# Optimization experiments

Measured on AMD Instinct MI355X. Metric: run time of the kernel, lower is better.

## Reference

```python
import jax, jax.numpy as jnp
import numpy as np

B, C, HF, WF = 32, 512, 8, 64   # pre-extracted VGG feature map
S = HF * WF                      # encoder sequence length = 512
T = 128                          # decode steps
V = 512                          # vocab size
E = 128                          # embedding dim
EH = 256                         # encoder hidden (per direction)
DH = 256                         # decoder hidden


def _p(key, shape, scale=0.08):
    return jax.random.normal(key, shape, dtype=jnp.float32) * scale


def setup_inputs() -> dict:
    key = jax.random.key(0)
    ks = jax.random.split(key, 24)
    inp = {
        'source': jax.random.normal(ks[0], (B, C, HF, WF), jnp.float32),
        'target': jax.random.randint(ks[1], (B, T), 0, V),
        # encoder bidirectional GRU (1 layer, input 512, hidden 256)
        'enc_Wih_f': _p(ks[2], (3 * EH, C)), 'enc_Whh_f': _p(ks[3], (3 * EH, EH)),
        'enc_bih_f': _p(ks[4], (3 * EH,)),   'enc_bhh_f': _p(ks[5], (3 * EH,)),
        'enc_Wih_b': _p(ks[6], (3 * EH, C)), 'enc_Whh_b': _p(ks[7], (3 * EH, EH)),
        'enc_bih_b': _p(ks[8], (3 * EH,)),   'enc_bhh_b': _p(ks[9], (3 * EH,)),
        # location-based attention: Linear(2*EH + DH -> 1)
        'att_W': _p(ks[10], (1, 2 * EH + DH)), 'att_b': _p(ks[11], (1,)),
        # decoder embedding
        'emb': _p(ks[12], (V, E), 0.1),
        # decoder GRU layer 0 (input E + 2*EH = 640 -> DH)
        'dec0_Wih': _p(ks[13], (3 * DH, E + 2 * EH)), 'dec0_Whh': _p(ks[14], (3 * DH, DH)),
        'dec0_bih': _p(ks[15], (3 * DH,)),            'dec0_bhh': _p(ks[16], (3 * DH,)),
        # decoder GRU layer 1 (DH -> DH)
        'dec1_Wih': _p(ks[17], (3 * DH, DH)), 'dec1_Whh': _p(ks[18], (3 * DH, DH)),
        'dec1_bih': _p(ks[19], (3 * DH,)),    'dec1_bhh': _p(ks[20], (3 * DH,)),
        # output layer DH -> V
        'out_W': _p(ks[21], (V, DH)), 'out_b': _p(ks[22], (V,)),
    }
    return inp


def gru_cell(x, h, Wih, Whh, bih, bhh):
    # PyTorch GRU cell semantics (gate order r, z, n)
    gi = x @ Wih.T + bih
    gh = h @ Whh.T + bhh
    ir, iz, inn = jnp.split(gi, 3, axis=-1)
    hr, hz, hn = jnp.split(gh, 3, axis=-1)
    r = jax.nn.sigmoid(ir + hr)
    z = jax.nn.sigmoid(iz + hz)
    n = jnp.tanh(inn + r * hn)
    return (1.0 - z) * n + z * h


def run_gru(xs, h0, Wih, Whh, bih, bhh):
    # xs: [S, B, D] -> outputs [S, B, H]
    def step(h, x):
        h2 = gru_cell(x, h, Wih, Whh, bih, bhh)
        return h2, h2
    _, ys = jax.lax.scan(step, h0, xs)
    return ys


def reference(source, target,
              enc_Wih_f, enc_Whh_f, enc_bih_f, enc_bhh_f,
              enc_Wih_b, enc_Whh_b, enc_bih_b, enc_bhh_b,
              att_W, att_b, emb,
              dec0_Wih, dec0_Whh, dec0_bih, dec0_bhh,
              dec1_Wih, dec1_Whh, dec1_bih, dec1_bhh,
              out_W, out_b):
    b, c, hf, wf = source.shape
    # features.view(b, c, -1).transpose(1, 2) -> [B, S, 512]
    seq = jnp.transpose(source.reshape(b, c, hf * wf), (0, 2, 1))
    xs = jnp.swapaxes(seq, 0, 1)  # [S, B, 512]

    h0 = jnp.zeros((b, EH), seq.dtype)
    ys_f = run_gru(xs, h0, enc_Wih_f, enc_Whh_f, enc_bih_f, enc_bhh_f)
    ys_b = run_gru(xs[::-1], h0, enc_Wih_b, enc_Whh_b, enc_bih_b, enc_bhh_b)[::-1]
    enc = jnp.swapaxes(jnp.concatenate([ys_f, ys_b], axis=-1), 0, 1)  # [B, S, 2*EH]

    ts = target.T  # [T, B]
    h_init = (jnp.zeros((b, DH), seq.dtype), jnp.zeros((b, DH), seq.dtype))

    def dec_step(carry, tok):
        h1, h2 = carry
        # attention over encoder outputs using last-layer hidden h2
        comb = jnp.concatenate(
            [enc, jnp.broadcast_to(h2[:, None, :], (b, enc.shape[1], DH))], axis=-1)
        scores = comb @ att_W.T + att_b          # [B, S, 1]
        w = jax.nn.softmax(scores, axis=1)
        ctx = jnp.sum(w * enc, axis=1)           # [B, 2*EH]
        x = jnp.concatenate([emb[tok], ctx], axis=-1)  # [B, E + 2*EH]
        h1n = gru_cell(x, h1, dec0_Wih, dec0_Whh, dec0_bih, dec0_bhh)
        h2n = gru_cell(h1n, h2, dec1_Wih, dec1_Whh, dec1_bih, dec1_bhh)
        out = h2n @ out_W.T + out_b              # [B, V]
        return (h1n, h2n), out

    _, outs = jax.lax.scan(dec_step, h_init, ts)  # [T, B, V]
    return jnp.swapaxes(outs, 0, 1)               # [B, T, V]
```

## Files before the change

### kernel.cpp

```cpp
#include <hip/hip_runtime.h>
#include <stdint.h>


typedef unsigned short u16;
typedef _Float16 h16;
typedef _Float16 f16x8 __attribute__((ext_vector_type(8)));
typedef float    f32x4 __attribute__((ext_vector_type(4)));

__device__ __forceinline__ f16x8 ld8(const h16* p){ return *reinterpret_cast<const f16x8*>(p); }
__device__ __forceinline__ f32x4 mfma16(f16x8 a, f16x8 b, f32x4 c){
  return __builtin_amdgcn_mfma_f32_16x16x32_f16(a, b, c, 0, 0, 0);
}
__device__ __forceinline__ float sigm(float x){ return 1.f/(1.f + __expf(-x)); }
__device__ __forceinline__ float tanhx(float x){ float e = __expf(2.f*x); return 1.f - 2.f/(e+1.f); }

__device__ __forceinline__ void gl_lds16(const void* g, void* l){
  __builtin_amdgcn_global_load_lds(
      (const __attribute__((address_space(1))) uint32_t*)g,
      (__attribute__((address_space(3))) uint32_t*)l, 16, 0, 0);
}

__device__ __forceinline__ void waitflag(int* f){
  while (__hip_atomic_load(f, __ATOMIC_RELAXED, __HIP_MEMORY_SCOPE_AGENT) == 0)
    __builtin_amdgcn_s_sleep(2);
  __builtin_amdgcn_fence(__ATOMIC_ACQUIRE, "agent");
}
__device__ __forceinline__ void post_flag(int* f, int tid){
  __builtin_amdgcn_fence(__ATOMIC_RELEASE, "agent");
  __syncthreads();
  if (tid == 0) __hip_atomic_store(f, 1, __ATOMIC_RELAXED, __HIP_MEMORY_SCOPE_AGENT);
}

__global__ __launch_bounds__(256) void k_transpose(const float* __restrict__ src,
                                                   h16* __restrict__ Xt){
  __shared__ h16 t[64][65];
  int blk = blockIdx.x;
  int b = blk >> 6, ct = (blk >> 3) & 7, st = blk & 7;
  int c0 = ct*64, s0 = st*64;
  int jj = threadIdx.x & 63, ii0 = threadIdx.x >> 6;
  for (int q = 0; q < 16; ++q){
    int i = ii0 + q*4;
    t[i][jj] = (h16)src[((size_t)(b*512 + c0 + i))*512 + s0 + jj];
  }
  __syncthreads();
  for (int q = 0; q < 16; ++q){
    int srow = ii0 + q*4;
    Xt[((size_t)((s0+srow)*32 + b))*512 + c0 + jj] = t[jj][srow];
  }
}

struct CastSegs {
  const float* src[11];
  h16* dst[11];
  int sstride[11];
  int lgr[11];
  int startblk[12];
};
__global__ __launch_bounds__(256) void k_cast(CastSegs cs){
  int blk = blockIdx.x;
  int seg = 0;
  while (seg < 10 && blk >= cs.startblk[seg+1]) ++seg;
  int base = (blk - cs.startblk[seg])*2048 + threadIdx.x*8;
  int lgr = cs.lgr[seg];
  int row = base >> lgr, col = base & ((1<<lgr)-1);
  const float* sp = cs.src[seg] + (size_t)row*cs.sstride[seg] + col;
  float4 v0 = reinterpret_cast<const float4*>(sp)[0];
  float4 v1 = reinterpret_cast<const float4*>(sp)[1];
  union { h16 o[8]; uint4 u; } pk;
  pk.o[0]=(h16)v0.x; pk.o[1]=(h16)v0.y; pk.o[2]=(h16)v0.z; pk.o[3]=(h16)v0.w;
  pk.o[4]=(h16)v1.x; pk.o[5]=(h16)v1.y; pk.o[6]=(h16)v1.z; pk.o[7]=(h16)v1.w;
  *reinterpret_cast<uint4*>(cs.dst[seg] + base) = pk.u;
}

__global__ __launch_bounds__(256) void k_bias(
    const float* eBihF, const float* eBhhF, const float* eBihB, const float* eBhhB,
    const float* d0bih, const float* d0bhh, const float* d1bih, const float* d1bhh,
    float* enc_bias, float* d0bias, float* d1bias){
  int tid = threadIdx.x;
  for (int i = tid; i < 1536; i += 256){
    bool bwd = i >= 768;
    int u = bwd ? i - 768 : i;
    float v = (bwd ? eBihB : eBihF)[u] + (u < 512 ? (bwd ? eBhhB : eBhhF)[u] : 0.f);
    enc_bias[i] = v;
  }
  for (int i = tid; i < 768; i += 256){
    d0bias[i] = d0bih[i] + (i < 512 ? d0bhh[i] : 0.f);
    d1bias[i] = d1bih[i] + (i < 512 ? d1bhh[i] : 0.f);
  }
}

struct GemmP {
  const h16* A; const h16* B; const float* bias;
  float* Cf; h16* Ch; float* Crm;
  int M, N, K, lda, ldb;
};
__global__ __launch_bounds__(256) void k_gemm(GemmP g){
  __shared__ __align__(16) h16 As[128*72];
  __shared__ __align__(16) h16 Bs[64*72];
  int tid = threadIdx.x, lane = tid & 63, wid = tid >> 6;
  int l15 = lane & 15, lg = lane >> 4;
  int m0 = blockIdx.y*128, n0 = blockIdx.x*64;
  int wm = wid & 1, wn = wid >> 1;
  f32x4 acc[4][2];
  for (int mt=0; mt<4; ++mt) for (int nt=0; nt<2; ++nt){ f32x4 z = {0.f,0.f,0.f,0.f}; acc[mt][nt] = z; }
  for (int k0 = 0; k0 < g.K; k0 += 64){
    for (int it = 0; it < 4; ++it){
      int c = tid + it*256; int row = c >> 3, kc = (c & 7)*8;
      uint4 v = {0,0,0,0};
      if (m0 + row < g.M) v = *reinterpret_cast<const uint4*>(g.A + (size_t)(m0+row)*g.lda + k0 + kc);
      *reinterpret_cast<uint4*>(&As[row*72 + kc]) = v;
    }
    for (int it = 0; it < 2; ++it){
      int c = tid + it*256; int row = c >> 3, kc = (c & 7)*8;
      uint4 v = *reinterpret_cast<const uint4*>(g.B + (size_t)(n0+row)*g.ldb + k0 + kc);
      *reinterpret_cast<uint4*>(&Bs[row*72 + kc]) = v;
    }
    __syncthreads();
    for (int kk = 0; kk < 2; ++kk){
      f16x8 a[4], bb[2];
      for (int mt=0; mt<4; ++mt) a[mt]  = ld8(&As[(wm*64 + mt*16 + l15)*72 + kk*32 + lg*8]);
      for (int nt=0; nt<2; ++nt) bb[nt] = ld8(&Bs[(wn*32 + nt*16 + l15)*72 + kk*32 + lg*8]);
      for (int mt=0; mt<4; ++mt) for (int nt=0; nt<2; ++nt)
        acc[mt][nt] = mfma16(a[mt], bb[nt], acc[mt][nt]);
    }
    __syncthreads();
  }
  for (int mt=0; mt<4; ++mt) for (int nt=0; nt<2; ++nt) for (int r=0; r<4; ++r){
    int m = m0 + wm*64 + mt*16 + 4*lg + r;
    int n = n0 + wn*32 + nt*16 + l15;
    if (m < g.M){
      float v = acc[mt][nt][r] + (g.bias ? g.bias[n] : 0.f);
      if (g.Cf) g.Cf[(size_t)m*g.N + n] = v;
      if (g.Ch) g.Ch[(size_t)m*g.N + n] = (h16)v;
      if (g.Crm) g.Crm[(size_t)(m & 31)*65536 + (size_t)(m >> 5)*512 + n] = v;
    }
  }
}

#define HSP 264
__global__ __launch_bounds__(512, 2) void k_enc_rnn(
    const h16* __restrict__ WhhF, const h16* __restrict__ WhhB,
    const float* __restrict__ bhhF, const float* __restrict__ bhhB,
    const h16* __restrict__ gi_enc,
    h16* __restrict__ enc)
{
  const int tid = threadIdx.x, lane = tid & 63, wid = tid >> 6;
  const int l15 = lane & 15, lg = lane >> 4;
  const int dir = blockIdx.x >> 1, half = blockIdx.x & 1, boff = half*16;
  const int j0 = wid*32;
  const h16* W = dir ? WhhB : WhhF;
  const float* bhh = dir ? bhhB : bhhF;

  __shared__ __align__(16) h16 hs[2][16*HSP];
  __shared__ __align__(16) h16 gis[2][16*768];

  f16x8 bw[3][2][8];
  #pragma unroll
  for (int gg=0; gg<3; ++gg) for (int jt=0; jt<2; ++jt) for (int kk=0; kk<8; ++kk)
    bw[gg][jt][kk] = ld8(W + (size_t)(gg*256 + j0 + jt*16 + l15)*256 + kk*32 + lg*8);
  float bhn[2] = { bhh[512 + j0 + l15], bhh[512 + j0 + 16 + l15] };
  float h_own[2][4] = {{0,0,0,0},{0,0,0,0}};
  for (int i = tid; i < 16*HSP; i += 512) hs[0][i] = (h16)0.f;
  {
    int s0 = dir ? 511 : 0;
    const h16* gb = gi_enc + (size_t)(s0*32 + boff)*1536 + dir*768;
    for (int q = 0; q < 3; ++q){
      int c = q*512 + tid;
      int row = c/96, col = (c%96)*8;
      gl_lds16(gb + (size_t)row*1536 + col, &gis[0][c*8]);
    }
  }
  __syncthreads();

  for (int p = 0; p < 512; ++p){
    const int cur = p & 1, nxt = cur ^ 1;
    const int s = dir ? (511 - p) : p;
    {
      int p2 = (p+1 < 512) ? p+1 : p;
      int s2 = dir ? (511 - p2) : p2;
      const h16* gb = gi_enc + (size_t)(s2*32 + boff)*1536 + dir*768;
      for (int q = 0; q < 3; ++q){
        int c = q*512 + tid;
        int row = c/96, col = (c%96)*8;
        gl_lds16(gb + (size_t)row*1536 + col, &gis[nxt][c*8]);
      }
    }
    f32x4 acc[3][2];
    #pragma unroll
    for (int jt=0; jt<2; ++jt)
      #pragma unroll
      for (int r=0; r<4; ++r){
        int b = 4*lg + r, u = j0 + jt*16 + l15;
        acc[0][jt][r] = (float)gis[cur][b*768 + u];
        acc[1][jt][r] = (float)gis[cur][b*768 + 256 + u];
        acc[2][jt][r] = jt ? bhn[1] : bhn[0];
      }
    f16x8 af[4];
    #pragma unroll
    for (int kk=0; kk<4; ++kk) af[kk] = ld8(&hs[cur][l15*HSP + kk*32 + lg*8]);
    #pragma unroll
    for (int kk=0; kk<4; ++kk)
      for (int gg=0; gg<3; ++gg) for (int jt=0; jt<2; ++jt)
        acc[gg][jt] = mfma16(af[kk], bw[gg][jt][kk], acc[gg][jt]);
    #pragma unroll
    for (int kk=0; kk<4; ++kk) af[kk] = ld8(&hs[cur][l15*HSP + (kk+4)*32 + lg*8]);
    #pragma unroll
    for (int kk=0; kk<4; ++kk)
      for (int gg=0; gg<3; ++gg) for (int jt=0; jt<2; ++jt)
        acc[gg][jt] = mfma16(af[kk], bw[gg][jt][kk+4], acc[gg][jt]);
    #pragma unroll
    for (int jt=0; jt<2; ++jt)
      for (int r=0; r<4; ++r){
        int b = 4*lg + r, j = j0 + jt*16 + l15;
        float gn = (float)gis[cur][b*768 + 512 + j];
        float rr = sigm(acc[0][jt][r]);
        float zz = sigm(acc[1][jt][r]);
        float nn = tanhx(gn + rr*acc[2][jt][r]);
        float hv = (1.f - zz)*nn + zz*h_own[jt][r];
        h_own[jt][r] = hv;
        h16 hb = (h16)hv;
        enc[((size_t)(boff + b)*512 + s)*512 + dir*256 + j] = hb;
        hs[nxt][b*HSP + j] = hb;
      }
    __syncthreads();
  }
}

__global__ __launch_bounds__(256) void k_attn(const h16* __restrict__ enc,
                                              const float* __restrict__ attW,
                                              h16* __restrict__ ctx_h){
  int b = blockIdx.x, tid = threadIdx.x;
  __shared__ float sc[512];
  __shared__ float red[8];
  const h16* eb = enc + (size_t)b*512*512;
  for (int sidx = tid; sidx < 512; sidx += 256){
    const h16* row = eb + (size_t)sidx*512;
    float acc = 0.f;
    for (int i = 0; i < 512; i += 4){
      acc += (float)row[i]*attW[i] + (float)row[i+1]*attW[i+1]
           + (float)row[i+2]*attW[i+2] + (float)row[i+3]*attW[i+3];
    }
    sc[sidx] = acc;
  }
  __syncthreads();
  float m = -1e30f;
  for (int i = tid; i < 512; i += 256) m = fmaxf(m, sc[i]);
  for (int off = 32; off > 0; off >>= 1) m = fmaxf(m, __shfl_down(m, off, 64));
  if (!(tid & 63)) red[tid >> 6] = m;
  __syncthreads();
  m = fmaxf(fmaxf(red[0], red[1]), fmaxf(red[2], red[3]));
  float sum = 0.f;
  for (int i = tid; i < 512; i += 256){ float e = __expf(sc[i] - m); sc[i] = e; sum += e; }
  for (int off = 32; off > 0; off >>= 1) sum += __shfl_down(sum, off, 64);
  if (!(tid & 63)) red[4 + (tid >> 6)] = sum;
  __syncthreads();
  float inv = 1.f / (red[4] + red[5] + red[6] + red[7]);
  float a0 = 0.f, a1 = 0.f;
  for (int s2 = 0; s2 < 512; ++s2){
    float w = sc[s2]*inv;
    a0 += w * (float)eb[(size_t)s2*512 + tid];
    a1 += w * (float)eb[(size_t)s2*512 + tid + 256];
  }
  ctx_h[b*512 + tid]       = (h16)a0;
  ctx_h[b*512 + tid + 256] = (h16)a1;
}

__global__ __launch_bounds__(512, 2) void k_dec_rnn(
    const h16* __restrict__ Whh0, const h16* __restrict__ Wih1, const h16* __restrict__ Whh1,
    const float* __restrict__ bhh0, const float* __restrict__ d1bias, const float* __restrict__ bhh1,
    const float* __restrict__ emb_all,
    const float* __restrict__ ctxp,
    const int* __restrict__ target,
    h16* __restrict__ h1n, float* __restrict__ gi2, h16* __restrict__ h2a,
    int* __restrict__ flagA, int* __restrict__ flagC)
{
  const int tid = threadIdx.x, lane = tid & 63, wid = tid >> 6;
  const int l15 = lane & 15, lg = lane >> 4;
  const int p = blockIdx.x & 1, kind = blockIdx.x >> 1;
  const int bg0 = p*16, j0 = wid*32;
  __shared__ __align__(16) h16 hs[2][16*HSP];

  if (kind == 0){
    f16x8 bw[3][2][8];
    for (int gg=0; gg<3; ++gg) for (int jt=0; jt<2; ++jt) for (int kk=0; kk<8; ++kk)
      bw[gg][jt][kk] = ld8(Whh0 + (size_t)(gg*256 + j0 + jt*16 + l15)*256 + kk*32 + lg*8);
    float bhn[2] = { bhh0[512 + j0 + l15], bhh0[512 + j0 + 16 + l15] };
    float h_own[2][4] = {{0,0,0,0},{0,0,0,0}};
    for (int i = tid; i < 16*HSP; i += 512) hs[0][i] = (h16)0.f;
    __syncthreads();
    for (int t = 0; t < 128; ++t){
      const int cur = t & 1, nxt = cur ^ 1;
      int tok[4];
      for (int r=0; r<4; ++r) tok[r] = target[(bg0 + 4*lg + r)*128 + t];
      f32x4 acc[3][2]; float gn[2][4];
      for (int jt=0; jt<2; ++jt){
        int u0 = j0 + jt*16 + l15;
        for (int r=0; r<4; ++r){
          const float* er = emb_all + (size_t)tok[r]*768;
          const float* cr = ctxp + (size_t)(bg0 + 4*lg + r)*768;
          acc[0][jt][r] = er[u0]       + cr[u0];
          acc[1][jt][r] = er[256 + u0] + cr[256 + u0];
          gn[jt][r]     = er[512 + u0] + cr[512 + u0];
          acc[2][jt][r] = bhn[jt];
        }
      }
      f16x8 af[4];
      for (int kk=0; kk<4; ++kk) af[kk] = ld8(&hs[cur][l15*HSP + kk*32 + lg*8]);
      for (int kk=0; kk<4; ++kk) for (int gg=0; gg<3; ++gg) for (int jt=0; jt<2; ++jt)
        acc[gg][jt] = mfma16(af[kk], bw[gg][jt][kk], acc[gg][jt]);
      for (int kk=0; kk<4; ++kk) af[kk] = ld8(&hs[cur][l15*HSP + (kk+4)*32 + lg*8]);
      for (int kk=0; kk<4; ++kk) for (int gg=0; gg<3; ++gg) for (int jt=0; jt<2; ++jt)
        acc[gg][jt] = mfma16(af[kk], bw[gg][jt][kk+4], acc[gg][jt]);
      for (int jt=0; jt<2; ++jt) for (int r=0; r<4; ++r){
        int b = 4*lg + r, j = j0 + jt*16 + l15;
        float rr = sigm(acc[0][jt][r]);
        float zz = sigm(acc[1][jt][r]);
        float nn = tanhx(gn[jt][r] + rr*acc[2][jt][r]);
        float hv = (1.f - zz)*nn + zz*h_own[jt][r];
        h_own[jt][r] = hv;
        h16 hb = (h16)hv;
        h1n[(size_t)(t*32 + bg0 + b)*256 + j] = hb;
        hs[nxt][b*HSP + j] = hb;
      }
      post_flag(&flagA[p*128 + t], tid);
    }
  } else if (kind == 1){
    f16x8 bw[3][2][8];
    for (int gg=0; gg<3; ++gg) for (int jt=0; jt<2; ++jt) for (int kk=0; kk<8; ++kk)
      bw[gg][jt][kk] = ld8(Wih1 + (size_t)(gg*256 + j0 + jt*16 + l15)*256 + kk*32 + lg*8);
    float bi[3][2];
    for (int gg=0; gg<3; ++gg) for (int jt=0; jt<2; ++jt) bi[gg][jt] = d1bias[gg*256 + j0 + jt*16 + l15];
    for (int t = 0; t < 128; ++t){
      waitflag(&flagA[p*128 + t]);
      const h16* hb = h1n + (size_t)(t*32 + bg0)*256;
      f32x4 acc[3][2];
      for (int gg=0; gg<3; ++gg) for (int jt=0; jt<2; ++jt) for (int r=0; r<4; ++r)
        acc[gg][jt][r] = bi[gg][jt];
      f16x8 af[4];
      for (int kk=0; kk<4; ++kk) af[kk] = ld8(hb + l15*256 + kk*32 + lg*8);
      for (int kk=0; kk<4; ++kk) for (int gg=0; gg<3; ++gg) for (int jt=0; jt<2; ++jt)
        acc[gg][jt] = mfma16(af[kk], bw[gg][jt][kk], acc[gg][jt]);
      for (int kk=0; kk<4; ++kk) af[kk] = ld8(hb + l15*256 + (kk+4)*32 + lg*8);
      for (int kk=0; kk<4; ++kk) for (int gg=0; gg<3; ++gg) for (int jt=0; jt<2; ++jt)
        acc[gg][jt] = mfma16(af[kk], bw[gg][jt][kk+4], acc[gg][jt]);
      for (int gg=0; gg<3; ++gg) for (int jt=0; jt<2; ++jt) for (int r=0; r<4; ++r){
        int b = 4*lg + r, u = gg*256 + j0 + jt*16 + l15;
        gi2[(size_t)(t*32 + bg0 + b)*768 + u] = acc[gg][jt][r];
      }
      post_flag(&flagC[p*128 + t], tid);
    }
  } else {
    f16x8 bw[3][2][8];
    for (int gg=0; gg<3; ++gg) for (int jt=0; jt<2; ++jt) for (int kk=0; kk<8; ++kk)
      bw[gg][jt][kk] = ld8(Whh1 + (size_t)(gg*256 + j0 + jt*16 + l15)*256 + kk*32 + lg*8);
    float bhn[2] = { bhh1[512 + j0 + l15], bhh1[512 + j0 + 16 + l15] };
    float h_own[2][4] = {{0,0,0,0},{0,0,0,0}};
    for (int i = tid; i < 16*HSP; i += 512) hs[0][i] = (h16)0.f;
    __syncthreads();
    for (int t = 0; t < 128; ++t){
      const int cur = t & 1, nxt = cur ^ 1;
      f32x4 acc[3][2];
      for (int gg=0; gg<3; ++gg) for (int jt=0; jt<2; ++jt) for (int r=0; r<4; ++r)
        acc[gg][jt][r] = (gg == 2) ? bhn[jt] : 0.f;
      f16x8 af[4];
      for (int kk=0; kk<4; ++kk) af[kk] = ld8(&hs[cur][l15*HSP + kk*32 + lg*8]);
      for (int kk=0; kk<4; ++kk) for (int gg=0; gg<3; ++gg) for (int jt=0; jt<2; ++jt)
        acc[gg][jt] = mfma16(af[kk], bw[gg][jt][kk], acc[gg][jt]);
      for (int kk=0; kk<4; ++kk) af[kk] = ld8(&hs[cur][l15*HSP + (kk+4)*32 + lg*8]);
      for (int kk=0; kk<4; ++kk) for (int gg=0; gg<3; ++gg) for (int jt=0; jt<2; ++jt)
        acc[gg][jt] = mfma16(af[kk], bw[gg][jt][kk+4], acc[gg][jt]);
      waitflag(&flagC[p*128 + t]);
      const float* g2 = gi2 + (size_t)(t*32 + bg0)*768;
      for (int jt=0; jt<2; ++jt) for (int r=0; r<4; ++r){
        int b = 4*lg + r, j = j0 + jt*16 + l15;
        float gr  = g2[(size_t)b*768 + j];
        float gz  = g2[(size_t)b*768 + 256 + j];
        float gnv = g2[(size_t)b*768 + 512 + j];
        float rr = sigm(gr + acc[0][jt][r]);
        float zz = sigm(gz + acc[1][jt][r]);
        float nn = tanhx(gnv + rr*acc[2][jt][r]);
        float hv = (1.f - zz)*nn + zz*h_own[jt][r];
        h_own[jt][r] = hv;
        h16 hb = (h16)hv;
        h2a[(size_t)(t*32 + bg0 + b)*256 + j] = hb;
        hs[nxt][b*HSP + j] = hb;
      }
      __syncthreads();
    }
  }
}

extern "C" void kernel_launch(void* const* d_in, const int* in_sizes, int n_in,
                              void* d_out, int out_size, void* d_ws, size_t ws_size,
                              hipStream_t stream){
  const float* source = (const float*)d_in[0];
  const int*   target = (const int*)  d_in[1];
  const float* eWihF = (const float*)d_in[2];
  const float* eWhhF = (const float*)d_in[3];
  const float* eBihF = (const float*)d_in[4];
  const float* eBhhF = (const float*)d_in[5];
  const float* eWihB = (const float*)d_in[6];
  const float* eWhhB = (const float*)d_in[7];
  const float* eBihB = (const float*)d_in[8];
  const float* eBhhB = (const float*)d_in[9];
  const float* attW  = (const float*)d_in[10];
  const float* emb   = (const float*)d_in[12];
  const float* d0Wih = (const float*)d_in[13];
  const float* d0Whh = (const float*)d_in[14];
  const float* d0bih = (const float*)d_in[15];
  const float* d0bhh = (const float*)d_in[16];
  const float* d1Wih = (const float*)d_in[17];
  const float* d1Whh = (const float*)d_in[18];
  const float* d1bih = (const float*)d_in[19];
  const float* d1bhh = (const float*)d_in[20];
  const float* outW  = (const float*)d_in[21];
  const float* outB  = (const float*)d_in[22];

  constexpr size_t OFF_XT   = 0;
  constexpr size_t OFF_GIE  = OFF_XT   + 16384ull*512*2;
  constexpr size_t OFF_ENC  = OFF_GIE  + 16384ull*1536*2;
  constexpr size_t OFF_WIHE = OFF_ENC  + 32ull*512*512*2;
  constexpr size_t OFF_WHHF = OFF_WIHE + 1536ull*512*2;
  constexpr size_t OFF_WHHB = OFF_WHHF + 768ull*256*2;
  constexpr size_t OFF_WHH0 = OFF_WHHB + 768ull*256*2;
  constexpr size_t OFF_WIH1 = OFF_WHH0 + 768ull*256*2;
  constexpr size_t OFF_WHH1 = OFF_WIH1 + 768ull*256*2;
  constexpr size_t OFF_OUTW = OFF_WHH1 + 768ull*256*2;
  constexpr size_t OFF_EMBB = OFF_OUTW + 512ull*256*2;
  constexpr size_t OFF_W0E  = OFF_EMBB + 512ull*128*2;
  constexpr size_t OFF_W0C  = OFF_W0E  + 768ull*128*2;
  constexpr size_t OFF_CTXB = OFF_W0C  + 768ull*512*2;
  constexpr size_t OFF_EMBA = OFF_CTXB + 32ull*512*2;
  constexpr size_t OFF_CTXP = OFF_EMBA + 512ull*768*4;
  constexpr size_t OFF_H1N  = OFF_CTXP + 32ull*768*4;
  constexpr size_t OFF_GI2  = OFF_H1N  + 128ull*32*256*2;
  constexpr size_t OFF_H2A  = OFF_GI2  + 128ull*32*768*4;
  constexpr size_t OFF_EBIA = OFF_H2A  + 128ull*32*256*2;
  constexpr size_t OFF_D0B  = OFF_EBIA + 1536*4;
  constexpr size_t OFF_D1B  = OFF_D0B  + 768*4;
  constexpr size_t OFF_FLG  = OFF_D1B  + 768*4;

  char* ws = (char*)d_ws;
  h16*   Xt      = (h16*)(ws + OFF_XT);
  h16*   gi_enc  = (h16*)(ws + OFF_GIE);
  h16*   ench    = (h16*)(ws + OFF_ENC);
  h16*   WihE    = (h16*)(ws + OFF_WIHE);
  h16*   WhhFh   = (h16*)(ws + OFF_WHHF);
  h16*   WhhBh   = (h16*)(ws + OFF_WHHB);
  h16*   Whh0h   = (h16*)(ws + OFF_WHH0);
  h16*   Wih1h   = (h16*)(ws + OFF_WIH1);
  h16*   Whh1h   = (h16*)(ws + OFF_WHH1);
  h16*   outWh   = (h16*)(ws + OFF_OUTW);
  h16*   embH    = (h16*)(ws + OFF_EMBB);
  h16*   W0E     = (h16*)(ws + OFF_W0E);
  h16*   W0C     = (h16*)(ws + OFF_W0C);
  h16*   ctxH    = (h16*)(ws + OFF_CTXB);
  float* emb_all = (float*)(ws + OFF_EMBA);
  float* ctxp    = (float*)(ws + OFF_CTXP);
  h16*   h1n     = (h16*)(ws + OFF_H1N);
  float* gi2     = (float*)(ws + OFF_GI2);
  h16*   h2a     = (h16*)(ws + OFF_H2A);
  float* ebias   = (float*)(ws + OFF_EBIA);
  float* d0bias  = (float*)(ws + OFF_D0B);
  float* d1bias  = (float*)(ws + OFF_D1B);
  int*   flagA   = (int*)(ws + OFF_FLG);
  int*   flagC   = flagA + 256;

  hipMemsetAsync(ws + OFF_FLG, 0, 2048, stream);
  k_transpose<<<2048, 256, 0, stream>>>(source, Xt);

  CastSegs cs;
  const float* srcs[11] = { eWihF, eWihB, eWhhF, eWhhB, d0Whh, d1Wih, d1Whh, outW, emb, d0Wih, d0Wih + 128 };
  h16* dsts[11] = { WihE, WihE + 768*512, WhhFh, WhhBh, Whh0h, Wih1h, Whh1h, outWh, embH, W0E, W0C };
  int strides[11] = { 512, 512, 256, 256, 256, 256, 256, 256, 128, 640, 640 };
  int lgrs[11]    = { 9,   9,   8,   8,   8,   8,   8,   8,   7,   7,   9 };
  int blks[11]    = { 192, 192, 96,  96,  96,  96,  96,  64,  32,  48,  192 };
  cs.startblk[0] = 0;
  for (int i = 0; i < 11; ++i){
    cs.src[i] = srcs[i]; cs.dst[i] = dsts[i]; cs.sstride[i] = strides[i]; cs.lgr[i] = lgrs[i];
    cs.startblk[i+1] = cs.startblk[i] + blks[i];
  }
  k_cast<<<1200, 256, 0, stream>>>(cs);
  k_bias<<<1, 256, 0, stream>>>(eBihF, eBhhF, eBihB, eBhhB, d0bih, d0bhh, d1bih, d1bhh,
                                ebias, d0bias, d1bias);

  GemmP ge; ge.A = Xt; ge.B = WihE; ge.bias = ebias; ge.Cf = nullptr; ge.Ch = gi_enc; ge.Crm = nullptr;
  ge.M = 16384; ge.N = 1536; ge.K = 512; ge.lda = 512; ge.ldb = 512;
  k_gemm<<<dim3(24, 128), 256, 0, stream>>>(ge);

  k_enc_rnn<<<4, 512, 0, stream>>>(WhhFh, WhhBh, eBhhF, eBhhB, gi_enc, ench);
  k_attn<<<32, 256, 0, stream>>>(ench, attW, ctxH);

  GemmP gc; gc.A = ctxH; gc.B = W0C; gc.bias = nullptr; gc.Cf = ctxp; gc.Ch = nullptr; gc.Crm = nullptr;
  gc.M = 32; gc.N = 768; gc.K = 512; gc.lda = 512; gc.ldb = 512;
  k_gemm<<<dim3(12, 1), 256, 0, stream>>>(gc);

  GemmP gm; gm.A = embH; gm.B = W0E; gm.bias = d0bias; gm.Cf = emb_all; gm.Ch = nullptr; gm.Crm = nullptr;
  gm.M = 512; gm.N = 768; gm.K = 128; gm.lda = 128; gm.ldb = 128;
  k_gemm<<<dim3(12, 4), 256, 0, stream>>>(gm);

  k_dec_rnn<<<6, 512, 0, stream>>>(Whh0h, Wih1h, Whh1h, d0bhh, d1bias, d1bhh,
                                   emb_all, ctxp, target, h1n, gi2, h2a, flagA, flagC);

  GemmP go; go.A = h2a; go.B = outWh; go.bias = outB; go.Cf = nullptr; go.Ch = nullptr; go.Crm = (float*)d_out;
  go.M = 4096; go.N = 512; go.K = 256; go.lda = 256; go.ldb = 256;
  k_gemm<<<dim3(8, 32), 256, 0, stream>>>(go);
}
```

Baseline: 3.237 ms.

## Restructure recurrent loops: direct gi loads, swizzled LDS hidden state, batched coalesced stores

The encoder RNN stops staging the gate inputs in LDS through async global-to-LDS copies. Each lane now loads its own gate values straight from global memory and adds them after the MFMA. The hidden state moves to an XOR-swizzled, unpadded LDS layout with 8 buffers, and encoder outputs are written in batches of 8 timesteps as coalesced 16-byte stores instead of scattered 2-byte stores. The decoder precomputes embedding plus context sums into an fp16 buffer in a new kernel, stores the gi2 intermediate in fp16, and writes h1/h2 with coalesced vector stores. Possible costs are global-load latency on the serial critical path and lower precision in the intermediates.

```diff
diff --git a/kernel.cpp b/kernel.cpp
--- a/kernel.cpp
+++ b/kernel.cpp
@@ -13,12 +13,6 @@
 }
 __device__ __forceinline__ float sigm(float x){ return 1.f/(1.f + __expf(-x)); }
 __device__ __forceinline__ float tanhx(float x){ float e = __expf(2.f*x); return 1.f - 2.f/(e+1.f); }
-
-__device__ __forceinline__ void gl_lds16(const void* g, void* l){
-  __builtin_amdgcn_global_load_lds(
-      (const __attribute__((address_space(1))) uint32_t*)g,
-      (__attribute__((address_space(3))) uint32_t*)l, 16, 0, 0);
-}
 
 __device__ __forceinline__ void waitflag(int* f){
   while (__hip_atomic_load(f, __ATOMIC_RELAXED, __HIP_MEMORY_SCOPE_AGENT) == 0)
@@ -137,7 +131,6 @@
   }
 }
 
-#define HSP 264
 __global__ __launch_bounds__(512, 2) void k_enc_rnn(
     const h16* __restrict__ WhhF, const h16* __restrict__ WhhB,
     const float* __restrict__ bhhF, const float* __restrict__ bhhB,
@@ -151,8 +144,7 @@
   const h16* W = dir ? WhhB : WhhF;
   const float* bhh = dir ? bhhB : bhhF;
 
-  __shared__ __align__(16) h16 hs[2][16*HSP];
-  __shared__ __align__(16) h16 gis[2][16*768];
+  __shared__ __align__(16) h16 hs[8][16*256];
 
   f16x8 bw[3][2][8];
   #pragma unroll
@@ -160,69 +152,62 @@
     bw[gg][jt][kk] = ld8(W + (size_t)(gg*256 + j0 + jt*16 + l15)*256 + kk*32 + lg*8);
   float bhn[2] = { bhh[512 + j0 + l15], bhh[512 + j0 + 16 + l15] };
   float h_own[2][4] = {{0,0,0,0},{0,0,0,0}};
-  for (int i = tid; i < 16*HSP; i += 512) hs[0][i] = (h16)0.f;
-  {
-    int s0 = dir ? 511 : 0;
-    const h16* gb = gi_enc + (size_t)(s0*32 + boff)*1536 + dir*768;
-    for (int q = 0; q < 3; ++q){
-      int c = q*512 + tid;
-      int row = c/96, col = (c%96)*8;
-      gl_lds16(gb + (size_t)row*1536 + col, &gis[0][c*8]);
-    }
-  }
+  for (int i = tid; i < 2048; i += 512) reinterpret_cast<uint32_t*>(hs[7])[i] = 0;
   __syncthreads();
 
+  const int s0 = dir ? 511 : 0;
+  const h16* gbase = gi_enc + (size_t)(s0*32 + boff)*1536 + dir*768 + j0 + l15;
+  const ptrdiff_t sstep = dir ? -(ptrdiff_t)(32*1536) : (ptrdiff_t)(32*1536);
+
   for (int p = 0; p < 512; ++p){
-    const int cur = p & 1, nxt = cur ^ 1;
-    const int s = dir ? (511 - p) : p;
-    {
-      int p2 = (p+1 < 512) ? p+1 : p;
-      int s2 = dir ? (511 - p2) : p2;
-      const h16* gb = gi_enc + (size_t)(s2*32 + boff)*1536 + dir*768;
-      for (int q = 0; q < 3; ++q){
-        int c = q*512 + tid;
-        int row = c/96, col = (c%96)*8;
-        gl_lds16(gb + (size_t)row*1536 + col, &gis[nxt][c*8]);
-      }
+    const int prev = (p+7)&7, cur = p&7;
+    h16 gv[3][2][4];
+    #pragma unroll
+    for (int r=0; r<4; ++r){
+      const h16* rp = gbase + (size_t)(4*lg + r)*1536;
+      #pragma unroll
+      for (int gg=0; gg<3; ++gg)
+        #pragma unroll
+        for (int jt=0; jt<2; ++jt)
+          gv[gg][jt][r] = rp[gg*256 + jt*16];
     }
     f32x4 acc[3][2];
     #pragma unroll
-    for (int jt=0; jt<2; ++jt)
-      #pragma unroll
-      for (int r=0; r<4; ++r){
-        int b = 4*lg + r, u = j0 + jt*16 + l15;
-        acc[0][jt][r] = (float)gis[cur][b*768 + u];
-        acc[1][jt][r] = (float)gis[cur][b*768 + 256 + u];
-        acc[2][jt][r] = jt ? bhn[1] : bhn[0];
-      }
-    f16x8 af[4];
+    for (int gg=0; gg<3; ++gg) for (int jt=0; jt<2; ++jt){ f32x4 z = {0.f,0.f,0.f,0.f}; acc[gg][jt] = z; }
     #pragma unroll
-    for (int kk=0; kk<4; ++kk) af[kk] = ld8(&hs[cur][l15*HSP + kk*32 + lg*8]);
-    #pragma unroll
-    for (int kk=0; kk<4; ++kk)
-      for (int gg=0; gg<3; ++gg) for (int jt=0; jt<2; ++jt)
-        acc[gg][jt] = mfma16(af[kk], bw[gg][jt][kk], acc[gg][jt]);
-    #pragma unroll
-    for (int kk=0; kk<4; ++kk) af[kk] = ld8(&hs[cur][l15*HSP + (kk+4)*32 + lg*8]);
-    #pragma unroll
-    for (int kk=0; kk<4; ++kk)
-      for (int gg=0; gg<3; ++gg) for (int jt=0; jt<2; ++jt)
-        acc[gg][jt] = mfma16(af[kk], bw[gg][jt][kk+4], acc[gg][jt]);
+    for (int kk=0; kk<8; ++kk){
+      f16x8 af = ld8(&hs[prev][l15*256 + ((kk*32 + lg*8) ^ ((l15&7)<<3))]);
+      #pragma unroll
+      for (int gg=0; gg<3; ++gg)
+        #pragma unroll
+        for (int jt=0; jt<2; ++jt)
+          acc[gg][jt] = mfma16(af, bw[gg][jt][kk], acc[gg][jt]);
+    }
     #pragma unroll
     for (int jt=0; jt<2; ++jt)
+      #pragma unroll
       for (int r=0; r<4; ++r){
-        int b = 4*lg + r, j = j0 + jt*16 + l15;
-        float gn = (float)gis[cur][b*768 + 512 + j];
-        float rr = sigm(acc[0][jt][r]);
-        float zz = sigm(acc[1][jt][r]);
-        float nn = tanhx(gn + rr*acc[2][jt][r]);
+        float rr = sigm((float)gv[0][jt][r] + acc[0][jt][r]);
+        float zz = sigm((float)gv[1][jt][r] + acc[1][jt][r]);
+        float nn = tanhx((float)gv[2][jt][r] + rr*(acc[2][jt][r] + bhn[jt]));
         float hv = (1.f - zz)*nn + zz*h_own[jt][r];
         h_own[jt][r] = hv;
-        h16 hb = (h16)hv;
-        enc[((size_t)(boff + b)*512 + s)*512 + dir*256 + j] = hb;
-        hs[nxt][b*HSP + j] = hb;
+        int b = 4*lg + r, j = j0 + jt*16 + l15;
+        hs[cur][b*256 + (j ^ ((b&7)<<3))] = (h16)hv;
       }
     __syncthreads();
+    if ((p & 7) == 7){
+      int b2 = tid >> 5, g2 = tid & 31;
+      #pragma unroll
+      for (int q2=0; q2<8; ++q2){
+        int pq = p - 7 + q2;
+        int s = dir ? (511 - pq) : pq;
+        uint4 v = *reinterpret_cast<const uint4*>(&hs[q2][b2*256 + 8*(g2 ^ (b2&7))]);
+        *reinterpret_cast<uint4*>(enc + ((size_t)((boff+b2)*512 + s))*512 + dir*256 + g2*8) = v;
+      }
+      __syncthreads();
+    }
+    gbase += sstep;
   }
 }
 
@@ -265,20 +250,33 @@
   ctx_h[b*512 + tid + 256] = (h16)a1;
 }
 
+__global__ __launch_bounds__(256) void k_xsum(const float* __restrict__ emb_all,
+                                              const float* __restrict__ ctxp,
+                                              const int* __restrict__ target,
+                                              h16* __restrict__ xsum){
+  int blk = blockIdx.x, t = blk >> 5, b = blk & 31, tid = threadIdx.x;
+  int tok = target[b*128 + t];
+  const float* er = emb_all + (size_t)tok*768;
+  const float* cr = ctxp + (size_t)b*768;
+  h16* out = xsum + (size_t)blk*768;
+  for (int q = 0; q < 3; ++q){
+    int u = tid + q*256;
+    out[u] = (h16)(er[u] + cr[u]);
+  }
+}
+
 __global__ __launch_bounds__(512, 2) void k_dec_rnn(
     const h16* __restrict__ Whh0, const h16* __restrict__ Wih1, const h16* __restrict__ Whh1,
     const float* __restrict__ bhh0, const float* __restrict__ d1bias, const float* __restrict__ bhh1,
-    const float* __restrict__ emb_all,
-    const float* __restrict__ ctxp,
-    const int* __restrict__ target,
-    h16* __restrict__ h1n, float* __restrict__ gi2, h16* __restrict__ h2a,
+    const h16* __restrict__ xsum,
+    h16* __restrict__ h1n, h16* __restrict__ gi2h, h16* __restrict__ h2a,
     int* __restrict__ flagA, int* __restrict__ flagC)
 {
   const int tid = threadIdx.x, lane = tid & 63, wid = tid >> 6;
   const int l15 = lane & 15, lg = lane >> 4;
   const int p = blockIdx.x & 1, kind = blockIdx.x >> 1;
   const int bg0 = p*16, j0 = wid*32;
-  __shared__ __align__(16) h16 hs[2][16*HSP];
+  __shared__ __align__(16) h16 hs[2][16*256];
 
   if (kind == 0){
     f16x8 bw[3][2][8];
@@ -286,42 +284,49 @@
       bw[gg][jt][kk] = ld8(Whh0 + (size_t)(gg*256 + j0 + jt*16 + l15)*256 + kk*32 + lg*8);
     float bhn[2] = { bhh0[512 + j0 + l15], bhh0[512 + j0 + 16 + l15] };
     float h_own[2][4] = {{0,0,0,0},{0,0,0,0}};
-    for (int i = tid; i < 16*HSP; i += 512) hs[0][i] = (h16)0.f;
+    for (int i = tid; i < 2048; i += 512) reinterpret_cast<uint32_t*>(hs[0])[i] = 0;
     __syncthreads();
     for (int t = 0; t < 128; ++t){
       const int cur = t & 1, nxt = cur ^ 1;
-      int tok[4];
-      for (int r=0; r<4; ++r) tok[r] = target[(bg0 + 4*lg + r)*128 + t];
-      f32x4 acc[3][2]; float gn[2][4];
-      for (int jt=0; jt<2; ++jt){
-        int u0 = j0 + jt*16 + l15;
+      const h16* xt = xsum + ((size_t)t*32 + bg0)*768 + j0 + l15;
+      h16 gv[3][2][4];
+      #pragma unroll
+      for (int r=0; r<4; ++r){
+        const h16* rp = xt + (size_t)(4*lg + r)*768;
+        #pragma unroll
+        for (int gg=0; gg<3; ++gg)
+          #pragma unroll
+          for (int jt=0; jt<2; ++jt)
+            gv[gg][jt][r] = rp[gg*256 + jt*16];
+      }
+      f32x4 acc[3][2];
+      #pragma unroll
+      for (int gg=0; gg<3; ++gg) for (int jt=0; jt<2; ++jt){ f32x4 z = {0.f,0.f,0.f,0.f}; acc[gg][jt] = z; }
+      #pragma unroll
+      for (int kk=0; kk<8; ++kk){
+        f16x8 af = ld8(&hs[cur][l15*256 + ((kk*32 + lg*8) ^ ((l15&7)<<3))]);
+        #pragma unroll
+        for (int gg=0; gg<3; ++gg)
+          #pragma unroll
+          for (int jt=0; jt<2; ++jt)
+            acc[gg][jt] = mfma16(af, bw[gg][jt][kk], acc[gg][jt]);
+      }
+      #pragma unroll
+      for (int jt=0; jt<2; ++jt)
+        #pragma unroll
         for (int r=0; r<4; ++r){
-          const float* er = emb_all + (size_t)tok[r]*768;
-          const float* cr = ctxp + (size_t)(bg0 + 4*lg + r)*768;
-          acc[0][jt][r] = er[u0]       + cr[u0];
-          acc[1][jt][r] = er[256 + u0] + cr[256 + u0];
-          gn[jt][r]     = er[512 + u0] + cr[512 + u0];
-          acc[2][jt][r] = bhn[jt];
+          float rr = sigm((float)gv[0][jt][r] + acc[0][jt][r]);
+          float zz = sigm((float)gv[1][jt][r] + acc[1][jt][r]);
+          float nn = tanhx((float)gv[2][jt][r] + rr*(acc[2][jt][r] + bhn[jt]));
+          float hv = (1.f - zz)*nn + zz*h_own[jt][r];
+          h_own[jt][r] = hv;
+          int b = 4*lg + r, j = j0 + jt*16 + l15;
+          hs[nxt][b*256 + (j ^ ((b&7)<<3))] = (h16)hv;
         }
-      }
-      f16x8 af[4];
-      for (int kk=0; kk<4; ++kk) af[kk] = ld8(&hs[cur][l15*HSP + kk*32 + lg*8]);
-      for (int kk=0; kk<4; ++kk) for (int gg=0; gg<3; ++gg) for (int jt=0; jt<2; ++jt)
-        acc[gg][jt] = mfma16(af[kk], bw[gg][jt][kk], acc[gg][jt]);
-      for (int kk=0; kk<4; ++kk) af[kk] = ld8(&hs[cur][l15*HSP + (kk+4)*32 + lg*8]);
-      for (int kk=0; kk<4; ++kk) for (int gg=0; gg<3; ++gg) for (int jt=0; jt<2; ++jt)
-        acc[gg][jt] = mfma16(af[kk], bw[gg][jt][kk+4], acc[gg][jt]);
-      for (int jt=0; jt<2; ++jt) for (int r=0; r<4; ++r){
-        int b = 4*lg + r, j = j0 + jt*16 + l15;
-        float rr = sigm(acc[0][jt][r]);
-        float zz = sigm(acc[1][jt][r]);
-        float nn = tanhx(gn[jt][r] + rr*acc[2][jt][r]);
-        float hv = (1.f - zz)*nn + zz*h_own[jt][r];
-        h_own[jt][r] = hv;
-        h16 hb = (h16)hv;
-        h1n[(size_t)(t*32 + bg0 + b)*256 + j] = hb;
-        hs[nxt][b*HSP + j] = hb;
-      }
+      __syncthreads();
+      { int b2 = tid >> 5, g2 = tid & 31;
+        uint4 v = *reinterpret_cast<const uint4*>(&hs[nxt][b2*256 + 8*(g2 ^ (b2&7))]);
+        *reinterpret_cast<uint4*>(h1n + ((size_t)t*32 + bg0 + b2)*256 + g2*8) = v; }
       post_flag(&flagA[p*128 + t], tid);
     }
   } else if (kind == 1){
@@ -334,18 +339,22 @@
       waitflag(&flagA[p*128 + t]);
       const h16* hb = h1n + (size_t)(t*32 + bg0)*256;
       f32x4 acc[3][2];
+      #pragma unroll
       for (int gg=0; gg<3; ++gg) for (int jt=0; jt<2; ++jt) for (int r=0; r<4; ++r)
         acc[gg][jt][r] = bi[gg][jt];
-      f16x8 af[4];
-      for (int kk=0; kk<4; ++kk) af[kk] = ld8(hb + l15*256 + kk*32 + lg*8);
-      for (int kk=0; kk<4; ++kk) for (int gg=0; gg<3; ++gg) for (int jt=0; jt<2; ++jt)
-        acc[gg][jt] = mfma16(af[kk], bw[gg][jt][kk], acc[gg][jt]);
-      for (int kk=0; kk<4; ++kk) af[kk] = ld8(hb + l15*256 + (kk+4)*32 + lg*8);
-      for (int kk=0; kk<4; ++kk) for (int gg=0; gg<3; ++gg) for (int jt=0; jt<2; ++jt)
-        acc[gg][jt] = mfma16(af[kk], bw[gg][jt][kk+4], acc[gg][jt]);
+      #pragma unroll
+      for (int kk=0; kk<8; ++kk){
+        f16x8 af = ld8(hb + l15*256 + kk*32 + lg*8);
+        #pragma unroll
+        for (int gg=0; gg<3; ++gg)
+          #pragma unroll
+          for (int jt=0; jt<2; ++jt)
+            acc[gg][jt] = mfma16(af, bw[gg][jt][kk], acc[gg][jt]);
+      }
+      #pragma unroll
       for (int gg=0; gg<3; ++gg) for (int jt=0; jt<2; ++jt) for (int r=0; r<4; ++r){
         int b = 4*lg + r, u = gg*256 + j0 + jt*16 + l15;
-        gi2[(size_t)(t*32 + bg0 + b)*768 + u] = acc[gg][jt][r];
+        gi2h[(size_t)(t*32 + bg0 + b)*768 + u] = (h16)acc[gg][jt][r];
       }
       post_flag(&flagC[p*128 + t], tid);
     }
@@ -355,36 +364,45 @@
       bw[gg][jt][kk] = ld8(Whh1 + (size_t)(gg*256 + j0 + jt*16 + l15)*256 + kk*32 + lg*8);
     float bhn[2] = { bhh1[512 + j0 + l15], bhh1[512 + j0 + 16 + l15] };
     float h_own[2][4] = {{0,0,0,0},{0,0,0,0}};
-    for (int i = tid; i < 16*HSP; i += 512) hs[0][i] = (h16)0.f;
+    for (int i = tid; i < 2048; i += 512) reinterpret_cast<uint32_t*>(hs[0])[i] = 0;
     __syncthreads();
     for (int t = 0; t < 128; ++t){
       const int cur = t & 1, nxt = cur ^ 1;
       f32x4 acc[3][2];
+      #pragma unroll
       for (int gg=0; gg<3; ++gg) for (int jt=0; jt<2; ++jt) for (int r=0; r<4; ++r)
         acc[gg][jt][r] = (gg == 2) ? bhn[jt] : 0.f;
-      f16x8 af[4];
-      for (int kk=0; kk<4; ++kk) af[kk] = ld8(&hs[cur][l15*HSP + kk*32 + lg*8]);
-      for (int kk=0; kk<4; ++kk) for (int gg=0; gg<3; ++gg) for (int jt=0; jt<2; ++jt)
-        acc[gg][jt] = mfma16(af[kk], bw[gg][jt][kk], acc[gg][jt]);
-      for (int kk=0; kk<4; ++kk) af[kk] = ld8(&hs[cur][l15*HSP + (kk+4)*32 + lg*8]);
-      for (int kk=0; kk<4; ++kk) for (int gg=0; gg<3; ++gg) for (int jt=0; jt<2; ++jt)
-        acc[gg][jt] = mfma16(af[kk], bw[gg][jt][kk+4], acc[gg][jt]);
+      #pragma unroll
+      for (int kk=0; kk<8; ++kk){
+        f16x8 af = ld8(&hs[cur][l15*256 + ((kk*32 + lg*8) ^ ((l15&7)<<3))]);
+        #pragma unroll
+        for (int gg=0; gg<3; ++gg)
+          #pragma unroll
+          for (int jt=0; jt<2; ++jt)
+            acc[gg][jt] = mfma16(af, bw[gg][jt][kk], acc[gg][jt]);
+      }
       waitflag(&flagC[p*128 + t]);
-      const float* g2 = gi2 + (size_t)(t*32 + bg0)*768;
-      for (int jt=0; jt<2; ++jt) for (int r=0; r<4; ++r){
-        int b = 4*lg + r, j = j0 + jt*16 + l15;
-        float gr  = g2[(size_t)b*768 + j];
-        float gz  = g2[(size_t)b*768 + 256 + j];
-        float gnv = g2[(size_t)b*768 + 512 + j];
-        float rr = sigm(gr + acc[0][jt][r]);
-        float zz = sigm(gz + acc[1][jt][r]);
-        float nn = tanhx(gnv + rr*acc[2][jt][r]);
-        float hv = (1.f - zz)*nn + zz*h_own[jt][r];
-        h_own[jt][r] = hv;
-        h16 hb = (h16)hv;
-        h2a[(size_t)(t*32 + bg0 + b)*256 + j] = hb;
-        hs[nxt][b*HSP + j] = hb;
-      }
+      const h16* g2p = gi2h + (size_t)(t*32 + bg0)*768 + j0 + l15;
+      #pragma unroll
+      for (int jt=0; jt<2; ++jt)
+        #pragma unroll
+        for (int r=0; r<4; ++r){
+          const h16* rp = g2p + (size_t)(4*lg + r)*768;
+          float gr  = (float)rp[jt*16];
+          float gz  = (float)rp[256 + jt*16];
+          float gnv = (float)rp[512 + jt*16];
+          float rr = sigm(gr + acc[0][jt][r]);
+          float zz = sigm(gz + acc[1][jt][r]);
+          float nn = tanhx(gnv + rr*acc[2][jt][r]);
+          float hv = (1.f - zz)*nn + zz*h_own[jt][r];
+          h_own[jt][r] = hv;
+          int b = 4*lg + r, j = j0 + jt*16 + l15;
+          hs[nxt][b*256 + (j ^ ((b&7)<<3))] = (h16)hv;
+        }
+      __syncthreads();
+      { int b2 = tid >> 5, g2 = tid & 31;
+        uint4 v = *reinterpret_cast<const uint4*>(&hs[nxt][b2*256 + 8*(g2 ^ (b2&7))]);
+        *reinterpret_cast<uint4*>(h2a + ((size_t)t*32 + bg0 + b2)*256 + g2*8) = v; }
       __syncthreads();
     }
   }
@@ -432,9 +450,10 @@
   constexpr size_t OFF_CTXB = OFF_W0C  + 768ull*512*2;
   constexpr size_t OFF_EMBA = OFF_CTXB + 32ull*512*2;
   constexpr size_t OFF_CTXP = OFF_EMBA + 512ull*768*4;
-  constexpr size_t OFF_H1N  = OFF_CTXP + 32ull*768*4;
+  constexpr size_t OFF_XSUM = OFF_CTXP + 32ull*768*4;
+  constexpr size_t OFF_H1N  = OFF_XSUM + 128ull*32*768*2;
   constexpr size_t OFF_GI2  = OFF_H1N  + 128ull*32*256*2;
-  constexpr size_t OFF_H2A  = OFF_GI2  + 128ull*32*768*4;
+  constexpr size_t OFF_H2A  = OFF_GI2  + 128ull*32*768*2;
   constexpr size_t OFF_EBIA = OFF_H2A  + 128ull*32*256*2;
   constexpr size_t OFF_D0B  = OFF_EBIA + 1536*4;
   constexpr size_t OFF_D1B  = OFF_D0B  + 768*4;
@@ -457,8 +476,9 @@
   h16*   ctxH    = (h16*)(ws + OFF_CTXB);
   float* emb_all = (float*)(ws + OFF_EMBA);
   float* ctxp    = (float*)(ws + OFF_CTXP);
+  h16*   xsum    = (h16*)(ws + OFF_XSUM);
   h16*   h1n     = (h16*)(ws + OFF_H1N);
-  float* gi2     = (float*)(ws + OFF_GI2);
+  h16*   gi2h    = (h16*)(ws + OFF_GI2);
   h16*   h2a     = (h16*)(ws + OFF_H2A);
   float* ebias   = (float*)(ws + OFF_EBIA);
   float* d0bias  = (float*)(ws + OFF_D0B);
@@ -499,8 +519,10 @@
   gm.M = 512; gm.N = 768; gm.K = 128; gm.lda = 128; gm.ldb = 128;
   k_gemm<<<dim3(12, 4), 256, 0, stream>>>(gm);
 
+  k_xsum<<<4096, 256, 0, stream>>>(emb_all, ctxp, target, xsum);
+
   k_dec_rnn<<<6, 512, 0, stream>>>(Whh0h, Wih1h, Whh1h, d0bhh, d1bias, d1bhh,
-                                   emb_all, ctxp, target, h1n, gi2, h2a, flagA, flagC);
+                                   xsum, h1n, gi2h, h2a, flagA, flagC);
 
   GemmP go; go.A = h2a; go.B = outWh; go.bias = outB; go.Cf = nullptr; go.Ch = nullptr; go.Crm = (float*)d_out;
   go.M = 4096; go.N = 512; go.K = 256; go.lda = 256; go.ldb = 256;
```

Result: slower. 4.047 ms (+25.0%).
